# Kernel optimization log

Hardware: AMD Instinct MI355X
Metric: run time of the kernel (lower is better)

The kernel has to match this reference:

```python
import jax, jax.numpy as jnp
import numpy as np

B, N, M = 16, 4096, 4096

def setup_inputs() -> dict:
    key = jax.random.key(0)
    k1, k2, k3 = jax.random.split(key, 3)
    src_points = jax.random.normal(k1, (B, N, 3), dtype=jnp.float32)
    tgt_points = jax.random.normal(k2, (B, M, 3), dtype=jnp.float32)
    weights = jax.random.uniform(k3, (B,), dtype=jnp.float32)
    return {"src_points": src_points, "tgt_points": tgt_points, "weights": weights}

def reference(src_points, tgt_points, weights):
    # Pairwise squared distances per batch: [B, N, M]
    # ||s - t||^2 = ||s||^2 + ||t||^2 - 2 s.t  (single dense intermediate)
    s2 = jnp.sum(src_points * src_points, axis=-1)  # [B, N]
    t2 = jnp.sum(tgt_points * tgt_points, axis=-1)  # [B, M]
    cross = jnp.einsum('bnd,bmd->bnm', src_points, tgt_points)  # [B, N, M]
    d2 = s2[:, :, None] + t2[:, None, :] - 2.0 * cross          # [B, N, M]
    d2 = jnp.maximum(d2, 0.0)  # numerical guard
    # Bidirectional chamfer: mean of nearest-neighbor squared distances
    d_src_to_tgt = jnp.mean(jnp.min(d2, axis=2), axis=1)  # [B]
    d_tgt_to_src = jnp.mean(jnp.min(d2, axis=1), axis=1)  # [B]
    distances = d_src_to_tgt + d_tgt_to_src               # [B]
    distances = distances * weights
    return jnp.mean(distances)  # reduction='mean'
```

## Files before the change

### kernel.cpp

```cpp
#include <hip/hip_runtime.h>

#define BQ 16
#define NP 4096
#define MP 4096

constexpr int TPB = 256;
constexpr int CHUNK = 256;
constexpr int SRC_PER_BLOCK = 128;

typedef __bf16 bf16x8 __attribute__((ext_vector_type(8)));
typedef float f32x16 __attribute__((ext_vector_type(16)));

union Frag {
    unsigned short u[8];
    bf16x8 v;
    int4 i4;
};

__device__ inline unsigned short f2bf(float f) {
    unsigned u = __float_as_uint(f);
    return (unsigned short)((u + 0x7FFFu + ((u >> 16) & 1u)) >> 16);
}
__device__ inline float bf2f(unsigned short h) {
    return __uint_as_float(((unsigned)h) << 16);
}

__global__ void chamfer_zero_kernel(float* __restrict__ out) { out[0] = 0.0f; }

__global__ __launch_bounds__(TPB) void chamfer_mfma_kernel(
    const float* __restrict__ srcp,
    const float* __restrict__ tgtp,
    const float* __restrict__ wts,
    float* __restrict__ out)
{
    const int gy  = blockIdx.y;
    const int dir = gy >> 4;
    const int b   = gy & 15;
    const float* S = dir ? (tgtp + (size_t)b * MP * 3) : (srcp + (size_t)b * NP * 3);
    const float* T = dir ? (srcp + (size_t)b * NP * 3) : (tgtp + (size_t)b * MP * 3);

    const int tid  = threadIdx.x;
    const int lane = tid & 63;
    const int half = lane >> 5;
    const int col  = lane & 31;
    const int wave = tid >> 6;

    __shared__ unsigned short sh[CHUNK * 16];
    __shared__ float partial[TPB / 64];

    const unsigned short ONE = 0x3F80;

    Frag bfrag;
    {
        const int sidx = blockIdx.x * SRC_PER_BLOCK + wave * 32 + col;
        const float* sp = S + (size_t)sidx * 3;
        float x = sp[0], y = sp[1], z = sp[2];
        unsigned short uh0 = f2bf(-2.0f * x), uh1 = f2bf(-2.0f * y), uh2 = f2bf(-2.0f * z);
        unsigned short ul0 = f2bf(-2.0f * x - bf2f(uh0));
        unsigned short ul1 = f2bf(-2.0f * y - bf2f(uh1));
        unsigned short ul2 = f2bf(-2.0f * z - bf2f(uh2));
        float s2 = fmaf(x, x, fmaf(y, y, z * z));
        unsigned short s2h = f2bf(s2), s2l = f2bf(s2 - bf2f(s2h));
        if (half == 0) {
            bfrag.u[0] = uh0; bfrag.u[1] = uh1; bfrag.u[2] = uh2;
            bfrag.u[3] = ul0; bfrag.u[4] = ul1; bfrag.u[5] = ul2;
            bfrag.u[6] = uh0; bfrag.u[7] = uh1;
        } else {
            bfrag.u[0] = uh2; bfrag.u[1] = ONE; bfrag.u[2] = ONE;
            bfrag.u[3] = s2h; bfrag.u[4] = s2l;
            bfrag.u[5] = 0;   bfrag.u[6] = 0;   bfrag.u[7] = 0;
        }
    }

    float accm = __int_as_float(0x7F800000);

    for (int c = 0; c < MP / CHUNK; ++c) {
        {
            const float* tp = T + (size_t)(c * CHUNK + tid) * 3;
            float x = tp[0], y = tp[1], z = tp[2];
            unsigned short xh = f2bf(x), yh = f2bf(y), zh = f2bf(z);
            unsigned short xl = f2bf(x - bf2f(xh));
            unsigned short yl = f2bf(y - bf2f(yh));
            unsigned short zl = f2bf(z - bf2f(zh));
            float t2 = fmaf(x, x, fmaf(y, y, z * z));
            unsigned short t2h = f2bf(t2), t2l = f2bf(t2 - bf2f(t2h));
            Frag p0, p1;
            p0.u[0] = xh; p0.u[1] = yh; p0.u[2] = zh;
            p0.u[3] = xh; p0.u[4] = yh; p0.u[5] = zh;
            p0.u[6] = xl; p0.u[7] = yl;
            p1.u[0] = zl;
            p1.u[1] = t2h; p1.u[2] = t2l;
            p1.u[3] = ONE; p1.u[4] = ONE;
            p1.u[5] = 0; p1.u[6] = 0; p1.u[7] = 0;
            const int sub = tid >> 5, row = tid & 31;
            *(int4*)&sh[sub * 512 + row * 8]       = p0.i4;
            *(int4*)&sh[sub * 512 + 256 + row * 8] = p1.i4;
        }
        __syncthreads();

#pragma unroll
        for (int sc = 0; sc < CHUNK / 32; ++sc) {
            Frag a;
            a.i4 = *(const int4*)&sh[sc * 512 + half * 256 + col * 8];
            f32x16 zc = {};
            f32x16 d = __builtin_amdgcn_mfma_f32_32x32x16_bf16(a.v, bfrag.v, zc, 0, 0, 0);
            float m0 = fminf(fminf(d[0], d[1]), d[2]);
            float m1 = fminf(fminf(d[3], d[4]), d[5]);
            float m2 = fminf(fminf(d[6], d[7]), d[8]);
            float m3 = fminf(fminf(d[9], d[10]), d[11]);
            float m4 = fminf(fminf(d[12], d[13]), d[14]);
            float t0 = fminf(fminf(m0, m1), m2);
            float t1 = fminf(fminf(m3, m4), d[15]);
            accm = fminf(fminf(accm, t0), t1);
        }
        __syncthreads();
    }

    float m = fminf(accm, __shfl_xor(accm, 32, 64));
    m = fmaxf(m, 0.0f);
#pragma unroll
    for (int off = 16; off > 0; off >>= 1) m += __shfl_xor(m, off, 64);
    if (lane == 0) partial[wave] = m;
    __syncthreads();
    if (tid == 0) {
        float v = partial[0] + partial[1] + partial[2] + partial[3];
        atomicAdd(out, v * wts[b] * (1.0f / ((float)NP * (float)BQ)));
    }
}

extern "C" void kernel_launch(void* const* d_in, const int* in_sizes, int n_in,
                              void* d_out, int out_size, void* d_ws, size_t ws_size,
                              hipStream_t stream) {
    const float* src = (const float*)d_in[0];
    const float* tgt = (const float*)d_in[1];
    const float* wts = (const float*)d_in[2];
    float* out = (float*)d_out;

    chamfer_zero_kernel<<<1, 1, 0, stream>>>(out);

    dim3 grid(NP / SRC_PER_BLOCK, 2 * BQ);
    chamfer_mfma_kernel<<<grid, TPB, 0, stream>>>(src, tgt, wts, out);
}
```

Baseline: 91.55 us.

## Precompute target fragments, reuse A across four source tiles, split targets over blocks

Adds a prep kernel that converts every point into the split-bf16 MFMA A-fragment layout once and stores it in a workspace table. The main kernel then copies prebuilt fragments into shared memory instead of redoing the conversion for each source block. Each wave now holds four source B-fragments, so every loaded A-fragment feeds four MFMAs. The target range is split across a grid dimension, with partial minima merged through atomicMin on float bits and summed in a separate reduce kernel. This costs two extra launches, a workspace round trip and global atomics, and falls back to the old kernel when the workspace is too small.

```diff
diff --git a/kernel.cpp b/kernel.cpp
--- a/kernel.cpp
+++ b/kernel.cpp
@@ -5,8 +5,11 @@
 #define MP 4096
 
 constexpr int TPB = 256;
+constexpr int WAVES = 4;
+constexpr int FR = 4;
+constexpr int SRC_PER_BLOCK = 32 * FR * WAVES;
+constexpr int TGT_PER_BLOCK = 1024;
 constexpr int CHUNK = 256;
-constexpr int SRC_PER_BLOCK = 128;
 
 typedef __bf16 bf16x8 __attribute__((ext_vector_type(8)));
 typedef float f32x16 __attribute__((ext_vector_type(16)));
@@ -25,19 +28,49 @@
     return __uint_as_float(((unsigned)h) << 16);
 }
 
-__global__ void chamfer_zero_kernel(float* __restrict__ out) { out[0] = 0.0f; }
-
-__global__ __launch_bounds__(TPB) void chamfer_mfma_kernel(
-    const float* __restrict__ srcp,
-    const float* __restrict__ tgtp,
-    const float* __restrict__ wts,
-    float* __restrict__ out)
-{
-    const int gy  = blockIdx.y;
-    const int dir = gy >> 4;
-    const int b   = gy & 15;
+__global__ __launch_bounds__(TPB) void chamfer_prep_kernel(
+    const float* __restrict__ srcp, const float* __restrict__ tgtp,
+    unsigned short* __restrict__ table, unsigned int* __restrict__ minbuf,
+    float* __restrict__ out) {
+    const int idx = blockIdx.x * TPB + threadIdx.x;
+    const int dir = idx >> 16;
+    const int rem = idx & 65535;
+    const float* rows = dir ? srcp : tgtp;
+    const float* p = rows + (size_t)rem * 3;
+    float x = p[0], y = p[1], z = p[2];
+    unsigned short xh = f2bf(x), yh = f2bf(y), zh = f2bf(z);
+    unsigned short xl = f2bf(x - bf2f(xh));
+    unsigned short yl = f2bf(y - bf2f(yh));
+    unsigned short zl = f2bf(z - bf2f(zh));
+    float t2 = fmaf(x, x, fmaf(y, y, z * z));
+    unsigned short t2h = f2bf(t2), t2l = f2bf(t2 - bf2f(t2h));
+    const unsigned short ONE = 0x3F80;
+    Frag p0, p1;
+    p0.u[0] = xh; p0.u[1] = yh; p0.u[2] = zh;
+    p0.u[3] = xh; p0.u[4] = yh; p0.u[5] = zh;
+    p0.u[6] = xl; p0.u[7] = yl;
+    p1.u[0] = zl;
+    p1.u[1] = t2h; p1.u[2] = t2l;
+    p1.u[3] = ONE; p1.u[4] = ONE;
+    p1.u[5] = 0; p1.u[6] = 0; p1.u[7] = 0;
+    int4* dst = (int4*)(table + (size_t)idx * 16);
+    dst[0] = p0.i4;
+    dst[1] = p1.i4;
+    minbuf[idx] = 0x7F800000u;
+    if (idx == 0) out[0] = 0.0f;
+}
+
+__global__ __launch_bounds__(TPB) void chamfer_main_kernel(
+    const float* __restrict__ srcp, const float* __restrict__ tgtp,
+    const unsigned short* __restrict__ table,
+    unsigned int* __restrict__ minbuf) {
+    const int gz  = blockIdx.z;
+    const int dir = gz >> 4;
+    const int b   = gz & 15;
     const float* S = dir ? (tgtp + (size_t)b * MP * 3) : (srcp + (size_t)b * NP * 3);
-    const float* T = dir ? (srcp + (size_t)b * NP * 3) : (tgtp + (size_t)b * MP * 3);
+    const unsigned short* At =
+        table + ((size_t)gz * 4096 + (size_t)blockIdx.y * TGT_PER_BLOCK) * 16;
+    unsigned int* mb = minbuf + (size_t)gz * 4096;
 
     const int tid  = threadIdx.x;
     const int lane = tid & 63;
@@ -46,13 +79,114 @@
     const int wave = tid >> 6;
 
     __shared__ unsigned short sh[CHUNK * 16];
-    __shared__ float partial[TPB / 64];
-
     const unsigned short ONE = 0x3F80;
 
+    Frag bf[FR];
+#pragma unroll
+    for (int f = 0; f < FR; ++f) {
+        const int sidx = blockIdx.x * SRC_PER_BLOCK + (wave * FR + f) * 32 + col;
+        const float* sp = S + (size_t)sidx * 3;
+        float x = sp[0], y = sp[1], z = sp[2];
+        unsigned short uh0 = f2bf(-2.0f * x), uh1 = f2bf(-2.0f * y), uh2 = f2bf(-2.0f * z);
+        unsigned short ul0 = f2bf(-2.0f * x - bf2f(uh0));
+        unsigned short ul1 = f2bf(-2.0f * y - bf2f(uh1));
+        unsigned short ul2 = f2bf(-2.0f * z - bf2f(uh2));
+        float s2 = fmaf(x, x, fmaf(y, y, z * z));
+        unsigned short s2h = f2bf(s2), s2l = f2bf(s2 - bf2f(s2h));
+        if (half == 0) {
+            bf[f].u[0] = uh0; bf[f].u[1] = uh1; bf[f].u[2] = uh2;
+            bf[f].u[3] = ul0; bf[f].u[4] = ul1; bf[f].u[5] = ul2;
+            bf[f].u[6] = uh0; bf[f].u[7] = uh1;
+        } else {
+            bf[f].u[0] = uh2; bf[f].u[1] = ONE; bf[f].u[2] = ONE;
+            bf[f].u[3] = s2h; bf[f].u[4] = s2l;
+            bf[f].u[5] = 0;   bf[f].u[6] = 0;  bf[f].u[7] = 0;
+        }
+    }
+
+    float accm[FR];
+#pragma unroll
+    for (int f = 0; f < FR; ++f) accm[f] = __int_as_float(0x7F800000);
+
+    const f32x16 zc = {};
+
+    for (int c = 0; c < TGT_PER_BLOCK / CHUNK; ++c) {
+        {
+            const int4* gp = (const int4*)(At + (size_t)c * CHUNK * 16);
+            int4* sp4 = (int4*)sh;
+            sp4[tid]       = gp[tid];
+            sp4[tid + 256] = gp[tid + 256];
+        }
+        __syncthreads();
+
+#pragma unroll
+        for (int sc = 0; sc < CHUNK / 32; ++sc) {
+            Frag a;
+            a.i4 = *(const int4*)&sh[sc * 512 + col * 16 + half * 8];
+#pragma unroll
+            for (int f = 0; f < FR; ++f) {
+                f32x16 d = __builtin_amdgcn_mfma_f32_32x32x16_bf16(a.v, bf[f].v, zc, 0, 0, 0);
+                float m0 = fminf(fminf(d[0], d[1]), d[2]);
+                float m1 = fminf(fminf(d[3], d[4]), d[5]);
+                float m2 = fminf(fminf(d[6], d[7]), d[8]);
+                float m3 = fminf(fminf(d[9], d[10]), d[11]);
+                float m4 = fminf(fminf(d[12], d[13]), d[14]);
+                float t0 = fminf(fminf(m0, m1), m2);
+                float t1 = fminf(fminf(m3, m4), d[15]);
+                accm[f] = fminf(fminf(accm[f], t0), t1);
+            }
+        }
+        __syncthreads();
+    }
+
+#pragma unroll
+    for (int f = 0; f < FR; ++f) {
+        float m = fminf(accm[f], __shfl_xor(accm[f], 32, 64));
+        m = fmaxf(m, 0.0f);
+        if (lane < 32) {
+            const int sidx = blockIdx.x * SRC_PER_BLOCK + (wave * FR + f) * 32 + col;
+            atomicMin(&mb[sidx], __float_as_uint(m));
+        }
+    }
+}
+
+__global__ __launch_bounds__(TPB) void chamfer_reduce_kernel(
+    const float* __restrict__ minbuf, const float* __restrict__ weights,
+    float* __restrict__ out) {
+    const int idx = blockIdx.x;
+    const int b = idx & 15;
+    const float* m0 = minbuf + (size_t)idx * 4096;
+
+    float s = 0.0f;
+    for (int i = threadIdx.x; i < 4096; i += TPB) s += m0[i];
+#pragma unroll
+    for (int off = 32; off > 0; off >>= 1) s += __shfl_down(s, off, 64);
+
+    __shared__ float red[TPB / 64];
+    if ((threadIdx.x & 63) == 0) red[threadIdx.x >> 6] = s;
+    __syncthreads();
+    if (threadIdx.x == 0) {
+        float tot = red[0] + red[1] + red[2] + red[3];
+        atomicAdd(out, weights[b] * tot * (1.0f / (4096.0f * (float)BQ)));
+    }
+}
+
+__global__ void chamfer_zero_kernel(float* __restrict__ out) { out[0] = 0.0f; }
+
+__global__ __launch_bounds__(TPB) void chamfer_mfma_fb_kernel(
+    const float* __restrict__ srcp, const float* __restrict__ tgtp,
+    const float* __restrict__ wts, float* __restrict__ out) {
+    const int gy = blockIdx.y, dir = gy >> 4, b = gy & 15;
+    const float* S = dir ? (tgtp + (size_t)b * MP * 3) : (srcp + (size_t)b * NP * 3);
+    const float* T = dir ? (srcp + (size_t)b * NP * 3) : (tgtp + (size_t)b * MP * 3);
+    const int tid = threadIdx.x, lane = tid & 63, half = lane >> 5,
+              col = tid & 31, wave = tid >> 6;
+    __shared__ unsigned short sh[256 * 16];
+    __shared__ float partial[4];
+    const unsigned short ONE = 0x3F80;
     Frag bfrag;
     {
-        const int sidx = blockIdx.x * SRC_PER_BLOCK + wave * 32 + col;
+        const int sidx = blockIdx.x * 128 + wave * 32 + (lane & 31);
         const float* sp = S + (size_t)sidx * 3;
         float x = sp[0], y = sp[1], z = sp[2];
         unsigned short uh0 = f2bf(-2.0f * x), uh1 = f2bf(-2.0f * y), uh2 = f2bf(-2.0f * z);
@@ -68,54 +202,46 @@
         } else {
             bfrag.u[0] = uh2; bfrag.u[1] = ONE; bfrag.u[2] = ONE;
             bfrag.u[3] = s2h; bfrag.u[4] = s2l;
-            bfrag.u[5] = 0;   bfrag.u[6] = 0;   bfrag.u[7] = 0;
-        }
-    }
-
+            bfrag.u[5] = 0;   bfrag.u[6] = 0;  bfrag.u[7] = 0;
+        }
+    }
     float accm = __int_as_float(0x7F800000);
-
-    for (int c = 0; c < MP / CHUNK; ++c) {
+    for (int c = 0; c < MP / 256; ++c) {
         {
-            const float* tp = T + (size_t)(c * CHUNK + tid) * 3;
+            const float* tp = T + (size_t)(c * 256 + tid) * 3;
             float x = tp[0], y = tp[1], z = tp[2];
             unsigned short xh = f2bf(x), yh = f2bf(y), zh = f2bf(z);
-            unsigned short xl = f2bf(x - bf2f(xh));
-            unsigned short yl = f2bf(y - bf2f(yh));
-            unsigned short zl = f2bf(z - bf2f(zh));
+            unsigned short xl = f2bf(x - bf2f(xh)), yl = f2bf(y - bf2f(yh)),
+                           zl = f2bf(z - bf2f(zh));
             float t2 = fmaf(x, x, fmaf(y, y, z * z));
             unsigned short t2h = f2bf(t2), t2l = f2bf(t2 - bf2f(t2h));
             Frag p0, p1;
             p0.u[0] = xh; p0.u[1] = yh; p0.u[2] = zh;
             p0.u[3] = xh; p0.u[4] = yh; p0.u[5] = zh;
             p0.u[6] = xl; p0.u[7] = yl;
-            p1.u[0] = zl;
-            p1.u[1] = t2h; p1.u[2] = t2l;
-            p1.u[3] = ONE; p1.u[4] = ONE;
-            p1.u[5] = 0; p1.u[6] = 0; p1.u[7] = 0;
+            p1.u[0] = zl; p1.u[1] = t2h; p1.u[2] = t2l;
+            p1.u[3] = ONE; p1.u[4] = ONE; p1.u[5] = 0; p1.u[6] = 0; p1.u[7] = 0;
             const int sub = tid >> 5, row = tid & 31;
-            *(int4*)&sh[sub * 512 + row * 8]       = p0.i4;
+            *(int4*)&sh[sub * 512 + row * 8] = p0.i4;
             *(int4*)&sh[sub * 512 + 256 + row * 8] = p1.i4;
         }
         __syncthreads();
-
-#pragma unroll
-        for (int sc = 0; sc < CHUNK / 32; ++sc) {
+        const f32x16 zc = {};
+#pragma unroll
+        for (int sc = 0; sc < 8; ++sc) {
             Frag a;
             a.i4 = *(const int4*)&sh[sc * 512 + half * 256 + col * 8];
-            f32x16 zc = {};
             f32x16 d = __builtin_amdgcn_mfma_f32_32x32x16_bf16(a.v, bfrag.v, zc, 0, 0, 0);
             float m0 = fminf(fminf(d[0], d[1]), d[2]);
             float m1 = fminf(fminf(d[3], d[4]), d[5]);
             float m2 = fminf(fminf(d[6], d[7]), d[8]);
             float m3 = fminf(fminf(d[9], d[10]), d[11]);
             float m4 = fminf(fminf(d[12], d[13]), d[14]);
-            float t0 = fminf(fminf(m0, m1), m2);
-            float t1 = fminf(fminf(m3, m4), d[15]);
-            accm = fminf(fminf(accm, t0), t1);
-        }
-        __syncthreads();
-    }
-
+            accm = fminf(accm, fminf(fminf(fminf(m0, m1), m2),
+                                     fminf(fminf(m3, m4), d[15])));
+        }
+        __syncthreads();
+    }
     float m = fminf(accm, __shfl_xor(accm, 32, 64));
     m = fmaxf(m, 0.0f);
 #pragma unroll
@@ -136,8 +262,24 @@
     const float* wts = (const float*)d_in[2];
     float* out = (float*)d_out;
 
-    chamfer_zero_kernel<<<1, 1, 0, stream>>>(out);
-
-    dim3 grid(NP / SRC_PER_BLOCK, 2 * BQ);
-    chamfer_mfma_kernel<<<grid, TPB, 0, stream>>>(src, tgt, wts, out);
-}
+    const size_t MINBUF_BYTES = (size_t)2 * BQ * 4096 * 4;
+    const size_t TABLE_BYTES  = (size_t)2 * BQ * 4096 * 32;
+
+    if (ws_size >= MINBUF_BYTES + TABLE_BYTES) {
+        unsigned int* minbuf = (unsigned int*)d_ws;
+        unsigned short* table = (unsigned short*)((char*)d_ws + MINBUF_BYTES);
+
+        chamfer_prep_kernel<<<(2 * BQ * 4096) / TPB, TPB, 0, stream>>>(
+            src, tgt, table, minbuf, out);
+
+        dim3 grid(NP / SRC_PER_BLOCK, MP / TGT_PER_BLOCK, 2 * BQ);
+        chamfer_main_kernel<<<grid, TPB, 0, stream>>>(src, tgt, table, minbuf);
+
+        chamfer_reduce_kernel<<<2 * BQ, TPB, 0, stream>>>(
+            (const float*)minbuf, wts, out);
+    } else {
+        chamfer_zero_kernel<<<1, 1, 0, stream>>>(out);
+        dim3 grid(NP / 128, 2 * BQ);
+        chamfer_mfma_fb_kernel<<<grid, TPB, 0, stream>>>(src, tgt, wts, out);
+    }
+}
```

New measurement: 93.37 us. Within noise of the previous version (+2.0%).
